# Kernel optimization log

Measured on AMD Instinct MI355X. Metric: run time of the kernel, lower is better.

## Reference

```python
import jax, jax.numpy as jnp
import numpy as np

B, S, D, F, T, NS, L, H = 8, 1024, 1024, 4096, 64, 512, 32, 16
TAG_RATE = 0.5      # config.tagging_rate
GSR = 0.5           # config.gate_scaling_rate
ATT_EPS = 1e-12     # config.layer_norm_eps (att_norm)
ENC_EPS = 1e-5      # torch TransformerEncoderLayer default


def _ln(x, g, b, eps):
    m = x.mean(-1, keepdims=True)
    v = x.var(-1, keepdims=True)
    return (x - m) * jax.lax.rsqrt(v + eps) * g + b


def _rope(x):
    # standard rotary embedding over the full hidden dim
    d = x.shape[-1]
    s = x.shape[1]
    inv = 1.0 / (10000.0 ** (jnp.arange(0, d, 2, dtype=jnp.float32) / d))
    ang = jnp.arange(s, dtype=jnp.float32)[:, None] * inv[None, :]  # [S, D/2]
    sin, cos = jnp.sin(ang), jnp.cos(ang)
    x1, x2 = x[..., 0::2], x[..., 1::2]
    return jnp.stack([x1 * cos - x2 * sin, x1 * sin + x2 * cos], axis=-1).reshape(x.shape)


def setup_inputs() -> dict:
    key = jax.random.key(0)
    ks = jax.random.split(key, 24)
    p = lambda k, shp: (0.02 * jax.random.normal(k, shp, dtype=jnp.float32))
    inp = {
        'word_embedding': jax.random.normal(ks[0], (B, S, D), dtype=jnp.float32),
        'attention_mask': jnp.ones((B, S), dtype=jnp.int32),
        'span_batch': jax.random.randint(ks[1], (NS,), 0, B, dtype=jnp.int32),
        'span_start': jax.random.randint(ks[2], (NS,), 0, S - L, dtype=jnp.int32),
        'span_tag': jax.random.randint(ks[3], (NS,), 0, T, dtype=jnp.int32),
        'tag_emb': p(ks[4], (T, D)),
        'gate_w': p(ks[5], (D, 1)),
        'gate_b': jnp.zeros((1,), jnp.float32),
        'attn_ln_g': jnp.ones((D,), jnp.float32),
        'attn_ln_b': jnp.zeros((D,), jnp.float32),
        'in_proj_w': p(ks[6], (3 * D, D)),
        'in_proj_b': jnp.zeros((3 * D,), jnp.float32),
        'out_proj_w': p(ks[7], (D, D)),
        'out_proj_b': jnp.zeros((D,), jnp.float32),
        'enc_ln1_g': jnp.ones((D,), jnp.float32),
        'enc_ln1_b': jnp.zeros((D,), jnp.float32),
        'lin1_w': p(ks[8], (F, D)),
        'lin1_b': jnp.zeros((F,), jnp.float32),
        'lin2_w': p(ks[9], (D, F)),
        'lin2_b': jnp.zeros((D,), jnp.float32),
        'enc_ln2_g': jnp.ones((D,), jnp.float32),
        'enc_ln2_b': jnp.zeros((D,), jnp.float32),
    }
    return inp


def _mha(x, pad, in_proj_w, in_proj_b, out_proj_w, out_proj_b):
    b, s, d = x.shape
    hd = d // H
    qkv = x @ in_proj_w.T + in_proj_b                       # [B,S,3D]
    q, k, v = jnp.split(qkv, 3, axis=-1)
    rs = lambda t: t.reshape(b, s, H, hd).transpose(0, 2, 1, 3)  # [B,H,S,hd]
    q, k, v = rs(q), rs(k), rs(v)
    scores = jnp.einsum('bhqd,bhkd->bhqk', q, k) / jnp.sqrt(jnp.float32(hd))
    scores = jnp.where(pad[:, None, None, :], jnp.float32(-1e30), scores)
    attn = jax.nn.softmax(scores, axis=-1)
    o = jnp.einsum('bhqk,bhkd->bhqd', attn, v).transpose(0, 2, 1, 3).reshape(b, s, d)
    return o @ out_proj_w.T + out_proj_b


def reference(word_embedding, attention_mask, span_batch, span_start, span_tag,
              tag_emb, gate_w, gate_b, attn_ln_g, attn_ln_b,
              in_proj_w, in_proj_b, out_proj_w, out_proj_b,
              enc_ln1_g, enc_ln1_b, lin1_w, lin1_b, lin2_w, lin2_b,
              enc_ln2_g, enc_ln2_b):
    raw = word_embedding                        # dropout off (eval)
    we = _rope(word_embedding)
    # ragged gather -> gate -> scatter-add over fixed-length spans
    tok = span_start[:, None] + jnp.arange(L, dtype=jnp.int32)[None, :]  # [NS,L]
    X = we[span_batch[:, None], tok]            # [NS,L,D]
    gate = GSR * jax.nn.sigmoid(X @ gate_w + gate_b) + (1.0 - GSR) / 2.0  # [NS,L,1]
    res = gate * tag_emb[span_tag][:, None, :] * jnp.float32(L)          # [NS,L,D]
    taged = jnp.zeros_like(word_embedding).at[span_batch[:, None], tok].add(res)
    out_emb = raw + taged * TAG_RATE            # if_merge_by_add
    out_emb = _ln(out_emb, attn_ln_g, attn_ln_b, ATT_EPS)
    pad = attention_mask == 0
    # torch TransformerEncoderLayer (post-norm, relu)
    a = _mha(out_emb, pad, in_proj_w, in_proj_b, out_proj_w, out_proj_b)
    x = _ln(out_emb + a, enc_ln1_g, enc_ln1_b, ENC_EPS)
    ff = jax.nn.relu(x @ lin1_w.T + lin1_b) @ lin2_w.T + lin2_b
    enc = _ln(x + ff, enc_ln2_g, enc_ln2_b, ENC_EPS)
    return enc + out_emb
```

## Files before the change

kernel.cpp:

```cpp
#include <hip/hip_runtime.h>

#define DEV __device__ __forceinline__

typedef short bf16x8 __attribute__((ext_vector_type(8)));
typedef float f32x4 __attribute__((ext_vector_type(4)));
typedef unsigned short u16;
typedef unsigned int u32;
typedef unsigned long long u64;

typedef __attribute__((address_space(3))) void lds_void;
typedef __attribute__((address_space(1))) void gbl_void;

DEV void async_copy16(void* lds_dst, const void* g_src) {
    __builtin_amdgcn_global_load_lds((gbl_void*)g_src, (lds_void*)lds_dst, 16, 0, 0);
}

DEV u16 f2bf(float x) {
    u32 u = __float_as_uint(x);
    return (u16)((u + 0x7fffu + ((u >> 16) & 1u)) >> 16);
}
DEV u16 f2bf_fast(float x) {
    return (u16)((__float_as_uint(x) + 0x8000u) >> 16);
}
DEV float bf2f(u16 v) { return __uint_as_float(((u32)v) << 16); }

__global__ __launch_bounds__(256) void prep_kernel(
    const float* __restrict__ we, const int* __restrict__ sb,
    const int* __restrict__ ss, const int* __restrict__ stg,
    const float* __restrict__ tag_emb, const float* __restrict__ gate_w,
    const float* __restrict__ gate_b, const float* __restrict__ g,
    const float* __restrict__ bta,
    const float* __restrict__ w0, const float* __restrict__ w1,
    const float* __restrict__ w2, const float* __restrict__ w3,
    u16* __restrict__ oe_bf, u16* __restrict__ o0, u16* __restrict__ o1,
    u16* __restrict__ o2, u16* __restrict__ o3) {
    const int blk = blockIdx.x;
    const int t = threadIdx.x;

    if (blk >= 8192) {
        int base = blk - 8192;
        const float* src; u16* dst;
        if (base < 3072)      { src = w0; dst = o0; }
        else if (base < 4096) { src = w1; dst = o1; base -= 3072; }
        else if (base < 8192) { src = w2; dst = o2; base -= 4096; }
        else                  { src = w3; dst = o3; base -= 8192; }
        const int i = base * 256 + t;
        const float4 v = ((const float4*)src)[i];
        ushort4 o;
        o.x = f2bf(v.x); o.y = f2bf(v.y); o.z = f2bf(v.z); o.w = f2bf(v.w);
        ((ushort4*)dst)[i] = o;
        return;
    }

    __shared__ float red[8];
    __shared__ u64 smask[8];
    const int row = blk;
    const int b = row >> 10;
    const int s = row & 1023;

    {
        const bool m0 = (sb[t] == b) && ((u32)(s - ss[t]) < 32u);
        const bool m1 = (sb[t + 256] == b) && ((u32)(s - ss[t + 256]) < 32u);
        const u64 b0 = __ballot(m0);
        const u64 b1 = __ballot(m1);
        if ((t & 63) == 0) { smask[t >> 6] = b0; smask[4 + (t >> 6)] = b1; }
    }

    float4 x = ((const float4*)(we + (long)row * 1024))[t];
    const float4 gw = ((const float4*)gate_w)[t];
    float dot;
    {
        const float p0 = (float)(2 * t);
        const float p1 = (float)(2 * t + 1);
        const float inv0 = exp2f(p0 * (-13.287712379549449f / 512.0f));
        const float inv1 = exp2f(p1 * (-13.287712379549449f / 512.0f));
        const float a0 = (float)s * inv0, a1 = (float)s * inv1;
        const float s0 = sinf(a0), c0 = cosf(a0);
        const float s1 = sinf(a1), c1 = cosf(a1);
        const float r1a = x.x * c0 - x.y * s0, r2a = x.x * s0 + x.y * c0;
        const float r1b = x.z * c1 - x.w * s1, r2b = x.z * s1 + x.w * c1;
        dot = r1a * gw.x + r2a * gw.y + r1b * gw.z + r2b * gw.w;
    }
#pragma unroll
    for (int off = 32; off > 0; off >>= 1) dot += __shfl_xor(dot, off, 64);
    if ((t & 63) == 0) red[t >> 6] = dot;
    __syncthreads();
    const float z = red[0] + red[1] + red[2] + red[3] + gate_b[0];
    const float gate = 0.25f + 0.5f / (1.f + __expf(-z));
    const float coef = gate * 16.f;

    float4 add = {0.f, 0.f, 0.f, 0.f};
#pragma unroll
    for (int gi = 0; gi < 8; ++gi) {
        u64 m = smask[gi];
        const int nb = (gi & 3) * 64 + (gi >> 2) * 256;
        while (m) {
            const int bit = __ffsll(m) - 1;
            m &= m - 1;
            const int tag = stg[nb + bit];
            const float4 te = ((const float4*)(tag_emb + (long)tag * 1024))[t];
            add.x += te.x; add.y += te.y; add.z += te.z; add.w += te.w;
        }
    }
    x.x += coef * add.x; x.y += coef * add.y;
    x.z += coef * add.z; x.w += coef * add.w;

    __syncthreads();
    float sm = x.x + x.y + x.z + x.w;
#pragma unroll
    for (int off = 32; off > 0; off >>= 1) sm += __shfl_xor(sm, off, 64);
    if ((t & 63) == 0) red[t >> 6] = sm;
    __syncthreads();
    const float mean = (red[0] + red[1] + red[2] + red[3]) * (1.f / 1024.f);
    float4 dx;
    dx.x = x.x - mean; dx.y = x.y - mean; dx.z = x.z - mean; dx.w = x.w - mean;
    float ss2 = dx.x * dx.x + dx.y * dx.y + dx.z * dx.z + dx.w * dx.w;
#pragma unroll
    for (int off = 32; off > 0; off >>= 1) ss2 += __shfl_xor(ss2, off, 64);
    if ((t & 63) == 0) red[4 + (t >> 6)] = ss2;
    __syncthreads();
    const float var = (red[4] + red[5] + red[6] + red[7]) * (1.f / 1024.f);
    const float rstd = rsqrtf(var + 1e-12f);
    const float4 gv = ((const float4*)g)[t];
    const float4 bv = ((const float4*)bta)[t];
    ushort4 o;
    o.x = f2bf(dx.x * rstd * gv.x + bv.x);
    o.y = f2bf(dx.y * rstd * gv.y + bv.y);
    o.z = f2bf(dx.z * rstd * gv.z + bv.z);
    o.w = f2bf(dx.w * rstd * gv.w + bv.w);
    ((ushort4*)(oe_bf + (long)row * 1024))[t] = o;
}

template <bool WRITE_F32, bool WRITE_BF, bool FINAL>
__global__ __launch_bounds__(256) void ln_kernel(
    const float* __restrict__ X, const float* __restrict__ g,
    const float* __restrict__ bta, float eps, float* __restrict__ Yf,
    u16* __restrict__ Ybf, const u16* __restrict__ addend) {
    __shared__ float red[8];
    const long row = blockIdx.x;
    const int t = threadIdx.x;
    const float4 x = ((const float4*)(X + row * 1024))[t];
    float s = x.x + x.y + x.z + x.w;
#pragma unroll
    for (int off = 32; off > 0; off >>= 1) s += __shfl_xor(s, off, 64);
    if ((t & 63) == 0) red[t >> 6] = s;
    __syncthreads();
    const float mean = (red[0] + red[1] + red[2] + red[3]) * (1.f / 1024.f);
    float4 dx;
    dx.x = x.x - mean; dx.y = x.y - mean; dx.z = x.z - mean; dx.w = x.w - mean;
    float ss = dx.x * dx.x + dx.y * dx.y + dx.z * dx.z + dx.w * dx.w;
#pragma unroll
    for (int off = 32; off > 0; off >>= 1) ss += __shfl_xor(ss, off, 64);
    if ((t & 63) == 0) red[4 + (t >> 6)] = ss;
    __syncthreads();
    const float var = (red[4] + red[5] + red[6] + red[7]) * (1.f / 1024.f);
    const float rstd = rsqrtf(var + eps);
    const float4 gv = ((const float4*)g)[t];
    const float4 bv = ((const float4*)bta)[t];
    float4 y;
    y.x = dx.x * rstd * gv.x + bv.x;
    y.y = dx.y * rstd * gv.y + bv.y;
    y.z = dx.z * rstd * gv.z + bv.z;
    y.w = dx.w * rstd * gv.w + bv.w;
    if (FINAL) {
        const ushort4 a = ((const ushort4*)(addend + row * 1024))[t];
        y.x += bf2f(a.x); y.y += bf2f(a.y); y.z += bf2f(a.z); y.w += bf2f(a.w);
    }
    if (WRITE_F32) ((float4*)(Yf + row * 1024))[t] = y;
    if (WRITE_BF) {
        ushort4 o;
        o.x = f2bf(y.x); o.y = f2bf(y.y); o.z = f2bf(y.z); o.w = f2bf(y.w);
        ((ushort4*)(Ybf + row * 1024))[t] = o;
    }
}

template <bool OUT_BF16, bool RELU, bool HAS_RES, bool VTRANS>
__global__ __launch_bounds__(256, 2) void gemm_nt(
    const u16* __restrict__ A, const u16* __restrict__ B,
    const float* __restrict__ bias, const u16* __restrict__ res,
    void* __restrict__ Cout, int N, int K, u16* __restrict__ vt) {
    __shared__ u16 Al[8192];
    __shared__ u16 Bl[8192];
    const int tid = threadIdx.x;
    const int wave = tid >> 6;
    const int lane = tid & 63;
    const int quad = lane >> 4;
    const int lq = lane & 15;
    const int wm = wave >> 1;
    const int wn = wave & 1;
    const long rowBase = (long)blockIdx.x * 128;
    const long colBase = (long)blockIdx.y * 128;

    f32x4 acc[4][4];
    const f32x4 fzero = {0.f, 0.f, 0.f, 0.f};
#pragma unroll
    for (int i = 0; i < 4; ++i)
#pragma unroll
        for (int j = 0; j < 4; ++j) acc[i][j] = fzero;

    const int rX = tid >> 3;
    const int pX = (tid & 7) ^ (rX & 7);
    const u16* gA = A + (rowBase + rX) * (long)K + pX * 8;
    const u16* gB = B + (colBase + rX) * (long)K + pX * 8;
    u16* ldsA = Al + wave * 512;
    u16* ldsB = Bl + wave * 512;

    for (int kt = 0; kt < K; kt += 64) {
        __syncthreads();
#pragma unroll
        for (int c = 0; c < 4; ++c) {
            async_copy16(ldsA + c * 2048, gA + (long)c * 32 * K + kt);
            async_copy16(ldsB + c * 2048, gB + (long)c * 32 * K + kt);
        }
        __syncthreads();
#pragma unroll
        for (int ks = 0; ks < 2; ++ks) {
            bf16x8 af[4], bfr[4];
#pragma unroll
            for (int i = 0; i < 4; ++i) {
                const int r = wm * 64 + i * 16 + lq;
                af[i] = *(const bf16x8*)&Al[r * 64 + (((ks * 4 + quad) ^ (lq & 7)) * 8)];
            }
#pragma unroll
            for (int j = 0; j < 4; ++j) {
                const int r = wn * 64 + j * 16 + lq;
                bfr[j] = *(const bf16x8*)&Bl[r * 64 + (((ks * 4 + quad) ^ (lq & 7)) * 8)];
            }
#pragma unroll
            for (int i = 0; i < 4; ++i)
#pragma unroll
                for (int j = 0; j < 4; ++j)
                    acc[i][j] = __builtin_amdgcn_mfma_f32_16x16x32_bf16(
                        af[i], bfr[j], acc[i][j], 0, 0, 0);
        }
    }

    float biasv[4];
#pragma unroll
    for (int j = 0; j < 4; ++j) biasv[j] = bias[colBase + wn * 64 + j * 16 + lq];
#pragma unroll
    for (int i = 0; i < 4; ++i) {
        const long grow = rowBase + wm * 64 + i * 16 + quad * 4;
#pragma unroll
        for (int j = 0; j < 4; ++j) {
            const long gcol = colBase + wn * 64 + j * 16 + lq;
#pragma unroll
            for (int r = 0; r < 4; ++r) {
                float v = acc[i][j][r] + biasv[j];
                if (RELU) v = fmaxf(v, 0.f);
                if (HAS_RES) v += bf2f(res[(grow + r) * N + gcol]);
                if (VTRANS && gcol >= 2048) {
                    const int hh = (int)(gcol - 2048) >> 6;
                    const int dd = (int)(gcol - 2048) & 63;
                    const long rr = grow + r;
                    const int bb = (int)(rr >> 10);
                    const int sR = (int)(rr & 1023);
                    vt[(((long)bb * 16 + hh) * 64 + dd) * 1024 + sR] = f2bf(v);
                } else if (OUT_BF16) {
                    ((u16*)Cout)[(grow + r) * N + gcol] = f2bf(v);
                } else {
                    ((float*)Cout)[(grow + r) * N + gcol] = v;
                }
            }
        }
    }
}

__global__ __launch_bounds__(256, 4) void attn_kernel(
    const u16* __restrict__ QKV, const u16* __restrict__ Vt,
    const int* __restrict__ mask, u16* __restrict__ Out) {
    __shared__ u16 KL[4096];
    __shared__ u16 VL[4096];
    __shared__ u16 PL[4][16 * 72];
    const int tid = threadIdx.x;
    const int wid = tid >> 6;
    const int lane = tid & 63;
    const int quad = lane >> 4;
    const int lq = lane & 15;
    const int slot0 = quad ^ (lq & 7);
    const int slot1 = slot0 ^ 4;

    const int bid = blockIdx.x;
    const int qb = bid & 7;
    const int h = (bid >> 3) & 15;
    const int b = bid >> 7;
    const int qbase = qb * 128 + wid * 32;

    bf16x8 aq[2][2];
#pragma unroll
    for (int t = 0; t < 2; ++t) {
        const u16* qp = QKV + ((long)(b * 1024 + qbase + t * 16 + lq)) * 3072 +
                        h * 64 + quad * 8;
        aq[t][0] = *(const bf16x8*)qp;
        aq[t][1] = *(const bf16x8*)(qp + 32);
    }

    const int c0 = tid, c1 = 256 + tid;
    const int r0 = c0 >> 3, j0 = (c0 & 7) ^ (r0 & 7);
    const int r1 = c1 >> 3, j1 = (c1 & 7) ^ (r1 & 7);
    const u16* srcK0 = QKV + ((long)(b * 1024 + r0)) * 3072 + 1024 + h * 64 + j0 * 8;
    const u16* srcK1 = QKV + ((long)(b * 1024 + r1)) * 3072 + 1024 + h * 64 + j1 * 8;
    const u16* srcV0 = Vt + ((long)(b * 16 + h) * 64 + r0) * 1024 + j0 * 8;
    const u16* srcV1 = Vt + ((long)(b * 16 + h) * 64 + r1) * 1024 + j1 * 8;
    u16* ldsK0 = KL + wid * 512;
    u16* ldsK1 = KL + 2048 + wid * 512;
    u16* ldsV0 = VL + wid * 512;
    u16* ldsV1 = VL + 2048 + wid * 512;

    const f32x4 fzero = {0.f, 0.f, 0.f, 0.f};
    f32x4 acc[2][4];
#pragma unroll
    for (int t = 0; t < 2; ++t)
#pragma unroll
        for (int j = 0; j < 4; ++j) acc[t][j] = fzero;
    float lsum[2][4] = {{0.f, 0.f, 0.f, 0.f}, {0.f, 0.f, 0.f, 0.f}};
    u16* myP = PL[wid];
    const int* mrow = mask + b * 1024;

    for (int kt = 0; kt < 1024; kt += 64) {
        __syncthreads();
        async_copy16(ldsK0, srcK0 + (long)kt * 3072);
        async_copy16(ldsK1, srcK1 + (long)kt * 3072);
        async_copy16(ldsV0, srcV0 + kt);
        async_copy16(ldsV1, srcV1 + kt);
        __syncthreads();

        bf16x8 kf0[4], kf1[4];
#pragma unroll
        for (int ct = 0; ct < 4; ++ct) {
            const int rowb = (ct * 16 + lq) * 64;
            kf0[ct] = *(const bf16x8*)&KL[rowb + slot0 * 8];
            kf1[ct] = *(const bf16x8*)&KL[rowb + slot1 * 8];
        }
        float mw[4];
#pragma unroll
        for (int ct = 0; ct < 4; ++ct) mw[ct] = mrow[kt + ct * 16 + lq] ? 1.f : 0.f;

#pragma unroll
        for (int t = 0; t < 2; ++t) {
            f32x4 s[4];
#pragma unroll
            for (int ct = 0; ct < 4; ++ct) {
                s[ct] = __builtin_amdgcn_mfma_f32_16x16x32_bf16(aq[t][0], kf0[ct],
                                                                fzero, 0, 0, 0);
                s[ct] = __builtin_amdgcn_mfma_f32_16x16x32_bf16(aq[t][1], kf1[ct],
                                                                s[ct], 0, 0, 0);
            }
            asm volatile("s_waitcnt lgkmcnt(0)" ::: "memory");
#pragma unroll
            for (int ct = 0; ct < 4; ++ct)
#pragma unroll
                for (int r = 0; r < 4; ++r) {
                    const float p = mw[ct] * __expf(s[ct][r] * 0.125f);
                    lsum[t][r] += p;
                    myP[(quad * 4 + r) * 72 + ct * 16 + lq] = f2bf_fast(p);
                }
            asm volatile("s_waitcnt lgkmcnt(0)" ::: "memory");
            const bf16x8 pf0 = *(const bf16x8*)&myP[lq * 72 + quad * 8];
            const bf16x8 pf1 = *(const bf16x8*)&myP[lq * 72 + 32 + quad * 8];
#pragma unroll
            for (int j = 0; j < 4; ++j) {
                const int rowb = (j * 16 + lq) * 64;
                const bf16x8 vf0 = *(const bf16x8*)&VL[rowb + slot0 * 8];
                const bf16x8 vf1 = *(const bf16x8*)&VL[rowb + slot1 * 8];
                acc[t][j] = __builtin_amdgcn_mfma_f32_16x16x32_bf16(pf0, vf0,
                                                                    acc[t][j], 0, 0, 0);
                acc[t][j] = __builtin_amdgcn_mfma_f32_16x16x32_bf16(pf1, vf1,
                                                                    acc[t][j], 0, 0, 0);
            }
        }
    }

#pragma unroll
    for (int t = 0; t < 2; ++t) {
        float inv[4];
#pragma unroll
        for (int r = 0; r < 4; ++r) {
            float l = lsum[t][r];
#pragma unroll
            for (int off = 1; off < 16; off <<= 1) l += __shfl_xor(l, off, 16);
            inv[r] = 1.f / l;
        }
        const long orow = (long)b * 1024 + qbase + t * 16 + quad * 4;
#pragma unroll
        for (int j = 0; j < 4; ++j)
#pragma unroll
            for (int r = 0; r < 4; ++r)
                Out[(orow + r) * 1024 + h * 64 + j * 16 + lq] =
                    f2bf_fast(acc[t][j][r] * inv[r]);
    }
}

extern "C" void kernel_launch(void* const* d_in, const int* in_sizes, int n_in,
                              void* d_out, int out_size, void* d_ws, size_t ws_size,
                              hipStream_t stream) {
    const float* we        = (const float*)d_in[0];
    const int*   amask     = (const int*)d_in[1];
    const int*   span_b    = (const int*)d_in[2];
    const int*   span_s    = (const int*)d_in[3];
    const int*   span_t    = (const int*)d_in[4];
    const float* tag_emb   = (const float*)d_in[5];
    const float* gate_w    = (const float*)d_in[6];
    const float* gate_b    = (const float*)d_in[7];
    const float* attn_ln_g = (const float*)d_in[8];
    const float* attn_ln_b = (const float*)d_in[9];
    const float* in_proj_w = (const float*)d_in[10];
    const float* in_proj_b = (const float*)d_in[11];
    const float* out_proj_w= (const float*)d_in[12];
    const float* out_proj_b= (const float*)d_in[13];
    const float* enc1_g    = (const float*)d_in[14];
    const float* enc1_b    = (const float*)d_in[15];
    const float* lin1_w    = (const float*)d_in[16];
    const float* lin1_b    = (const float*)d_in[17];
    const float* lin2_w    = (const float*)d_in[18];
    const float* lin2_b    = (const float*)d_in[19];
    const float* enc2_g    = (const float*)d_in[20];
    const float* enc2_b    = (const float*)d_in[21];
    float* out = (float*)d_out;

    char* ws = (char*)d_ws;
    size_t off = 0;
    auto alloc = [&](size_t bytes) {
        void* p = ws + off;
        off += (bytes + 255) & ~(size_t)255;
        return p;
    };
    const size_t MT = 8192;
    u16* oe_bf   = (u16*)alloc(MT * 1024 * 2);
    u16* ax_bf   = (u16*)alloc(MT * 1024 * 2);
    char* region = (char*)alloc((size_t)67108864);
    u16* qkv_bf  = (u16*)region;
    u16* vt_bf   = (u16*)(region + (size_t)MT * 3072 * 2);
    u16* ff1_bf  = (u16*)region;
    u16* wb_inproj  = (u16*)alloc((size_t)3072 * 1024 * 2);
    u16* wb_outproj = (u16*)alloc((size_t)1024 * 1024 * 2);
    u16* wb_lin1    = (u16*)alloc((size_t)4096 * 1024 * 2);
    u16* wb_lin2    = (u16*)alloc((size_t)1024 * 4096 * 2);

    prep_kernel<<<20480, 256, 0, stream>>>(
        we, span_b, span_s, span_t, tag_emb, gate_w, gate_b,
        attn_ln_g, attn_ln_b, in_proj_w, out_proj_w, lin1_w, lin2_w,
        oe_bf, wb_inproj, wb_outproj, wb_lin1, wb_lin2);
    dim3 g1(64, 24);
    gemm_nt<true, false, false, true><<<g1, 256, 0, stream>>>(
        oe_bf, wb_inproj, in_proj_b, nullptr, qkv_bf, 3072, 1024, vt_bf);
    attn_kernel<<<1024, 256, 0, stream>>>(qkv_bf, vt_bf, amask, ax_bf);
    dim3 g2(64, 8);
    gemm_nt<false, false, true, false><<<g2, 256, 0, stream>>>(
        ax_bf, wb_outproj, out_proj_b, oe_bf, out, 1024, 1024, nullptr);
    ln_kernel<false, true, false><<<8192, 256, 0, stream>>>(
        out, enc1_g, enc1_b, 1e-5f, nullptr, ax_bf, nullptr);
    dim3 g3(64, 32);
    gemm_nt<true, true, false, false><<<g3, 256, 0, stream>>>(
        ax_bf, wb_lin1, lin1_b, nullptr, ff1_bf, 4096, 1024, nullptr);
    gemm_nt<false, false, true, false><<<g2, 256, 0, stream>>>(
        ff1_bf, wb_lin2, lin2_b, ax_bf, out, 1024, 4096, nullptr);
    ln_kernel<true, false, true><<<8192, 256, 0, stream>>>(
        out, enc2_g, enc2_b, 1e-5f, out, nullptr, oe_bf);
}
```

Before: 483.8 us.

## Keep attention probabilities in registers via transposed QK MFMA and lane shuffles

The QK^T MFMA now takes its operands in swapped order, so each lane holds a transposed score tile. The probabilities are packed to bf16 pairs and moved into the PV A-operand layout with cross-lane shuffles. This removes the per-wave LDS staging buffer for P, along with its write, wait and read round trip. Row sums are reduced with shuffles, and the mask is loaded as int4. In exchange the kernel issues many ds_bpermute shuffles, which still use the LDS hardware path.

```diff
diff --git a/kernel.cpp b/kernel.cpp
--- a/kernel.cpp
+++ b/kernel.cpp
@@ -23,6 +23,9 @@
     return (u16)((__float_as_uint(x) + 0x8000u) >> 16);
 }
 DEV float bf2f(u16 v) { return __uint_as_float(((u32)v) << 16); }
+DEV u32 packbf2(float a, float b) {
+    return (u32)f2bf_fast(a) | ((u32)f2bf_fast(b) << 16);
+}
 
 __global__ __launch_bounds__(256) void prep_kernel(
     const float* __restrict__ we, const int* __restrict__ sb,
@@ -271,7 +274,6 @@
     const int* __restrict__ mask, u16* __restrict__ Out) {
     __shared__ u16 KL[4096];
     __shared__ u16 VL[4096];
-    __shared__ u16 PL[4][16 * 72];
     const int tid = threadIdx.x;
     const int wid = tid >> 6;
     const int lane = tid & 63;
@@ -313,9 +315,12 @@
     for (int t = 0; t < 2; ++t)
 #pragma unroll
         for (int j = 0; j < 4; ++j) acc[t][j] = fzero;
-    float lsum[2][4] = {{0.f, 0.f, 0.f, 0.f}, {0.f, 0.f, 0.f, 0.f}};
-    u16* myP = PL[wid];
+    float lsumq[2] = {0.f, 0.f};
     const int* mrow = mask + b * 1024;
+
+    const int sl0 = lq + ((quad & 1) << 5);
+    const int sl1 = sl0 + 16;
+    const bool hi = (quad >> 1) != 0;
 
     for (int kt = 0; kt < 1024; kt += 64) {
         __syncthreads();
@@ -332,40 +337,71 @@
             kf0[ct] = *(const bf16x8*)&KL[rowb + slot0 * 8];
             kf1[ct] = *(const bf16x8*)&KL[rowb + slot1 * 8];
         }
-        float mw[4];
-#pragma unroll
-        for (int ct = 0; ct < 4; ++ct) mw[ct] = mrow[kt + ct * 16 + lq] ? 1.f : 0.f;
+        float mwv[4][4];
+#pragma unroll
+        for (int ct = 0; ct < 4; ++ct) {
+            const int4 m4 = *(const int4*)&mrow[kt + ct * 16 + quad * 4];
+            mwv[ct][0] = m4.x ? 1.f : 0.f;
+            mwv[ct][1] = m4.y ? 1.f : 0.f;
+            mwv[ct][2] = m4.z ? 1.f : 0.f;
+            mwv[ct][3] = m4.w ? 1.f : 0.f;
+        }
 
 #pragma unroll
         for (int t = 0; t < 2; ++t) {
             f32x4 s[4];
 #pragma unroll
             for (int ct = 0; ct < 4; ++ct) {
-                s[ct] = __builtin_amdgcn_mfma_f32_16x16x32_bf16(aq[t][0], kf0[ct],
+                s[ct] = __builtin_amdgcn_mfma_f32_16x16x32_bf16(kf0[ct], aq[t][0],
                                                                 fzero, 0, 0, 0);
-                s[ct] = __builtin_amdgcn_mfma_f32_16x16x32_bf16(aq[t][1], kf1[ct],
+                s[ct] = __builtin_amdgcn_mfma_f32_16x16x32_bf16(kf1[ct], aq[t][1],
                                                                 s[ct], 0, 0, 0);
             }
-            asm volatile("s_waitcnt lgkmcnt(0)" ::: "memory");
-#pragma unroll
-            for (int ct = 0; ct < 4; ++ct)
-#pragma unroll
-                for (int r = 0; r < 4; ++r) {
-                    const float p = mw[ct] * __expf(s[ct][r] * 0.125f);
-                    lsum[t][r] += p;
-                    myP[(quad * 4 + r) * 72 + ct * 16 + lq] = f2bf_fast(p);
-                }
-            asm volatile("s_waitcnt lgkmcnt(0)" ::: "memory");
-            const bf16x8 pf0 = *(const bf16x8*)&myP[lq * 72 + quad * 8];
-            const bf16x8 pf1 = *(const bf16x8*)&myP[lq * 72 + 32 + quad * 8];
+            u32 W[4][2];
+            float ls = 0.f;
+#pragma unroll
+            for (int ct = 0; ct < 4; ++ct) {
+                const float p0 = mwv[ct][0] * __expf(s[ct][0] * 0.125f);
+                const float p1 = mwv[ct][1] * __expf(s[ct][1] * 0.125f);
+                const float p2 = mwv[ct][2] * __expf(s[ct][2] * 0.125f);
+                const float p3 = mwv[ct][3] * __expf(s[ct][3] * 0.125f);
+                ls += (p0 + p1) + (p2 + p3);
+                W[ct][0] = packbf2(p0, p1);
+                W[ct][1] = packbf2(p2, p3);
+            }
+            ls += __shfl_xor(ls, 16, 64);
+            ls += __shfl_xor(ls, 32, 64);
+            lsumq[t] += ls;
+
+            union { u32 w[4]; bf16x8 v; } pf0u, pf1u;
+            {
+                u32 a, c;
+                a = __shfl((int)W[0][0], sl0, 64); c = __shfl((int)W[1][0], sl0, 64);
+                pf0u.w[0] = hi ? c : a;
+                a = __shfl((int)W[0][1], sl0, 64); c = __shfl((int)W[1][1], sl0, 64);
+                pf0u.w[1] = hi ? c : a;
+                a = __shfl((int)W[0][0], sl1, 64); c = __shfl((int)W[1][0], sl1, 64);
+                pf0u.w[2] = hi ? c : a;
+                a = __shfl((int)W[0][1], sl1, 64); c = __shfl((int)W[1][1], sl1, 64);
+                pf0u.w[3] = hi ? c : a;
+                a = __shfl((int)W[2][0], sl0, 64); c = __shfl((int)W[3][0], sl0, 64);
+                pf1u.w[0] = hi ? c : a;
+                a = __shfl((int)W[2][1], sl0, 64); c = __shfl((int)W[3][1], sl0, 64);
+                pf1u.w[1] = hi ? c : a;
+                a = __shfl((int)W[2][0], sl1, 64); c = __shfl((int)W[3][0], sl1, 64);
+                pf1u.w[2] = hi ? c : a;
+                a = __shfl((int)W[2][1], sl1, 64); c = __shfl((int)W[3][1], sl1, 64);
+                pf1u.w[3] = hi ? c : a;
+            }
+
 #pragma unroll
             for (int j = 0; j < 4; ++j) {
                 const int rowb = (j * 16 + lq) * 64;
                 const bf16x8 vf0 = *(const bf16x8*)&VL[rowb + slot0 * 8];
                 const bf16x8 vf1 = *(const bf16x8*)&VL[rowb + slot1 * 8];
-                acc[t][j] = __builtin_amdgcn_mfma_f32_16x16x32_bf16(pf0, vf0,
+                acc[t][j] = __builtin_amdgcn_mfma_f32_16x16x32_bf16(pf0u.v, vf0,
                                                                     acc[t][j], 0, 0, 0);
-                acc[t][j] = __builtin_amdgcn_mfma_f32_16x16x32_bf16(pf1, vf1,
+                acc[t][j] = __builtin_amdgcn_mfma_f32_16x16x32_bf16(pf1u.v, vf1,
                                                                     acc[t][j], 0, 0, 0);
             }
         }
@@ -375,12 +411,8 @@
     for (int t = 0; t < 2; ++t) {
         float inv[4];
 #pragma unroll
-        for (int r = 0; r < 4; ++r) {
-            float l = lsum[t][r];
-#pragma unroll
-            for (int off = 1; off < 16; off <<= 1) l += __shfl_xor(l, off, 16);
-            inv[r] = 1.f / l;
-        }
+        for (int r = 0; r < 4; ++r)
+            inv[r] = 1.f / __shfl(lsumq[t], quad * 4 + r, 16);
         const long orow = (long)b * 1024 + qbase + t * 16 + quad * 4;
 #pragma unroll
         for (int j = 0; j < 4; ++j)
```

Result: slower. 522.9 us (+8.1%).
